# Performance work log

Hardware: AMD Instinct MI355X
Metric: run time of the kernel (lower is better)

The kernel has to match this reference:

```python
import jax, jax.numpy as jnp
import numpy as np

DIM = 96       # d_model / channels
DSTATE = 16    # SSM state size N
DINNER = 2 * DIM   # expand=2 -> 192
DTRANK = 6     # ceil(DIM/16)
K = 4          # scan directions
B, H, W = 2, 56, 56


def _ln(x, g, b, eps=1e-5):
    m = x.mean(-1, keepdims=True)
    v = x.var(-1, keepdims=True)
    return (x - m) * jax.lax.rsqrt(v + eps) * g + b


def _dwconv3(x, w, b):  # x [B,C,H,W], w [C,1,3,3] depthwise, SAME padding
    y = jax.lax.conv_general_dilated(x, w, (1, 1), [(1, 1), (1, 1)],
                                     feature_group_count=x.shape[1],
                                     dimension_numbers=('NCHW', 'OIHW', 'NCHW'))
    return y + b[None, :, None, None]


def _bn(x, g, b, m, v, eps=1e-5):  # eval-mode BatchNorm2d on NCHW
    inv = jax.lax.rsqrt(v + eps)
    return (x - m[None, :, None, None]) * (inv * g)[None, :, None, None] + b[None, :, None, None]


def _selective_scan(u, dt, A, Bs, Cs, Dp, dt_bias):
    # u, dt: [B,K,D,L]; A: [K,D,N]; Bs,Cs: [B,K,N,L]; Dp, dt_bias: [K,D]
    dt = jax.nn.softplus(dt + dt_bias[None, :, :, None])
    dA = jnp.exp(jnp.einsum('bkdl,kdn->lbkdn', dt, A))           # [L,B,K,D,N]
    dBu = jnp.einsum('bkdl,bknl,bkdl->lbkdn', dt, Bs, u)          # [L,B,K,D,N]
    Ct = jnp.moveaxis(Cs, -1, 0)                                  # [L,B,K,N]
    h0 = jnp.zeros(dA.shape[1:], dA.dtype)

    def step(h, inp):
        dA_l, dBu_l, C_l = inp
        h = dA_l * h + dBu_l
        return h, jnp.einsum('bkdn,bkn->bkd', h, C_l)

    _, ys = jax.lax.scan(step, h0, (dA, dBu, Ct))                 # ys [L,B,K,D]
    return jnp.moveaxis(ys, 0, -1) + u * Dp[None, :, :, None]     # [B,K,D,L]


def setup_inputs() -> dict:
    key = jax.random.key(0)
    ks = jax.random.split(key, 12)
    s = 0.02
    f32 = jnp.float32
    inp = {}
    inp['x'] = jax.random.normal(ks[0], (B, H, W, DIM), f32)
    # conv branch: depthwise 3x3 + BN + ReLU + 1x1 + BN
    inp['dw_w'] = jax.random.normal(ks[1], (DIM, 1, 3, 3), f32) * s
    inp['dw_b'] = jnp.zeros((DIM,), f32)
    inp['bn1_g'] = jnp.ones((DIM,), f32); inp['bn1_b'] = jnp.zeros((DIM,), f32)
    inp['bn1_m'] = jnp.zeros((DIM,), f32); inp['bn1_v'] = jnp.ones((DIM,), f32)
    inp['pw_w'] = jax.random.normal(ks[2], (DIM, DIM), f32) * s
    inp['pw_b'] = jnp.zeros((DIM,), f32)
    inp['bn2_g'] = jnp.ones((DIM,), f32); inp['bn2_b'] = jnp.zeros((DIM,), f32)
    inp['bn2_m'] = jnp.zeros((DIM,), f32); inp['bn2_v'] = jnp.ones((DIM,), f32)
    # pre-mamba LayerNorm
    inp['ln_g'] = jnp.ones((DIM,), f32); inp['ln_b'] = jnp.zeros((DIM,), f32)
    # SS2D params
    inp['in_proj_w'] = jax.random.normal(ks[3], (2 * DINNER, DIM), f32) * s
    inp['conv_w'] = jax.random.normal(ks[4], (DINNER, 1, 3, 3), f32) * s
    inp['conv_b'] = jnp.zeros((DINNER,), f32)
    inp['x_proj_w'] = jax.random.normal(ks[5], (K, DTRANK + 2 * DSTATE, DINNER), f32) * s
    inp['dt_w'] = jax.random.normal(ks[6], (K, DINNER, DTRANK), f32) * s
    inp['dt_b'] = jnp.full((K, DINNER), -4.6, f32)  # softplus(dt_b) ~= 0.01
    inp['A_logs'] = jnp.log(jnp.tile(jnp.arange(1, DSTATE + 1, dtype=f32), (K * DINNER, 1)))
    inp['Ds'] = jnp.ones((K * DINNER,), f32)
    inp['out_norm_g'] = jnp.ones((DINNER,), f32); inp['out_norm_b'] = jnp.zeros((DINNER,), f32)
    inp['out_proj_w'] = jax.random.normal(ks[7], (DIM, DINNER), f32) * s
    # fusion: Linear(2*dim, dim) + LayerNorm(dim)
    inp['fus_w'] = jax.random.normal(ks[8], (DIM, 2 * DIM), f32) * s
    inp['fus_b'] = jnp.zeros((DIM,), f32)
    inp['fus_ln_g'] = jnp.ones((DIM,), f32); inp['fus_ln_b'] = jnp.zeros((DIM,), f32)
    return inp


def reference(x, dw_w, dw_b, bn1_g, bn1_b, bn1_m, bn1_v, pw_w, pw_b,
              bn2_g, bn2_b, bn2_m, bn2_v, ln_g, ln_b,
              in_proj_w, conv_w, conv_b, x_proj_w, dt_w, dt_b, A_logs, Ds,
              out_norm_g, out_norm_b, out_proj_w, fus_w, fus_b, fus_ln_g, fus_ln_b):
    Bsz, Hh, Ww, C = x.shape
    L = Hh * Ww
    # ----- conv branch -----
    xc = jnp.transpose(x, (0, 3, 1, 2))                       # [B,C,H,W]
    c = jax.nn.relu(_bn(_dwconv3(xc, dw_w, dw_b), bn1_g, bn1_b, bn1_m, bn1_v))
    c = jnp.einsum('bchw,oc->bohw', c, pw_w) + pw_b[None, :, None, None]
    conv_out = jnp.transpose(_bn(c, bn2_g, bn2_b, bn2_m, bn2_v), (0, 2, 3, 1))
    # ----- mamba (SS2D) branch -----
    xn = _ln(x, ln_g, ln_b)
    xz = xn @ in_proj_w.T                                     # [B,H,W,2*Din]
    xm, z = jnp.split(xz, 2, axis=-1)
    xm = jnp.transpose(xm, (0, 3, 1, 2))                      # [B,Din,H,W]
    xm = jax.nn.silu(_dwconv3(xm, conv_w, conv_b))
    v1 = xm.reshape(Bsz, DINNER, L)                           # row-major scan
    v2 = jnp.transpose(xm, (0, 1, 3, 2)).reshape(Bsz, DINNER, L)  # col-major scan
    xs = jnp.stack([v1, v2, v1[..., ::-1], v2[..., ::-1]], axis=1)  # [B,4,Din,L]
    x_dbl = jnp.einsum('bkdl,kcd->bkcl', xs, x_proj_w)
    dts, Bmat, Cmat = jnp.split(x_dbl, [DTRANK, DTRANK + DSTATE], axis=2)
    dts = jnp.einsum('bkrl,kdr->bkdl', dts, dt_w)
    A = -jnp.exp(A_logs).reshape(K, DINNER, DSTATE)
    out_y = _selective_scan(xs, dts, A, Bmat, Cmat, Ds.reshape(K, DINNER), dt_b)
    y1 = out_y[:, 0]
    inv_y = out_y[:, 2:4][..., ::-1]
    y2 = inv_y[:, 0]
    y3 = jnp.transpose(inv_y[:, 1].reshape(Bsz, DINNER, Ww, Hh), (0, 1, 3, 2)).reshape(Bsz, DINNER, L)
    y4 = jnp.transpose(out_y[:, 1].reshape(Bsz, DINNER, Ww, Hh), (0, 1, 3, 2)).reshape(Bsz, DINNER, L)
    y = jnp.transpose(y1 + y2 + y3 + y4, (0, 2, 1)).reshape(Bsz, Hh, Ww, DINNER)
    y = _ln(y, out_norm_g, out_norm_b)
    y = y * jax.nn.silu(z)
    mamba_out = y @ out_proj_w.T                              # [B,H,W,C]
    # ----- fusion + residual -----
    fused = jnp.concatenate([conv_out, mamba_out], axis=-1) @ fus_w.T + fus_b
    fused = _ln(fused, fus_ln_g, fus_ln_b)
    return x + fused
```

## Files before the change

kernel.cpp:

```cpp
#include <hip/hip_runtime.h>
#include <math.h>

#define BZ 2
#define HH 56
#define WW 56
#define LL 3136
#define CC 96
#define DI 192
#define NS 16
#define RR 6
#define NT 49
#define NCH 98
#define CH 32

#define OFF_CONV   0
#define OFF_XMRAW  602112
#define OFF_Z      1806336
#define OFF_V1     3010560
#define OFF_V2     4214784
#define OFF_DT     5419008
#define OFF_BS     10235904
#define OFF_CS     10637312
#define OFF_Y      11038720
#define OFF_Y13    15855616
#define OFF_T      18264064
#define OFF_W2     19468288

__device__ __forceinline__ float softplusf(float x) {
    if (x > 20.f) return x;
    return log1pf(__expf(x));
}

__global__ __launch_bounds__(64) void k0_w2(const float* __restrict__ fus_w,
                                            const float* __restrict__ opw,
                                            float* __restrict__ W2) {
    int i = blockIdx.x * 64 + threadIdx.x;
    if (i >= CC * DI) return;
    int o = i / DI, d = i % DI;
    float acc = 0.f;
    for (int j = 0; j < CC; ++j)
        acc += fus_w[o * DI + CC + j] * opw[j * DI + d];
    W2[i] = acc;
}

__global__ __launch_bounds__(256) void k0c_negA(const float* __restrict__ A_logs,
                                                float* __restrict__ negA) {
    int i = blockIdx.x * 256 + threadIdx.x;
    if (i < 4 * DI * NS) negA[i] = -__expf(A_logs[i]);
}

__global__ __launch_bounds__(256) void k1a_dw(const float* __restrict__ x,
    const float* __restrict__ dw_w, const float* __restrict__ dw_b,
    const float* __restrict__ bn1_g, const float* __restrict__ bn1_b,
    const float* __restrict__ bn1_m, const float* __restrict__ bn1_v,
    float* __restrict__ cbuf) {
    int i = blockIdx.x * 256 + threadIdx.x;
    if (i >= BZ * LL * CC) return;
    int c = i % CC;
    int bl = i / CC;
    int l = bl % LL, b = bl / LL;
    int h = l / WW, w = l % WW;
    float acc = dw_b[c];
    #pragma unroll
    for (int dy = -1; dy <= 1; ++dy) {
        int hh = h + dy; if (hh < 0 || hh >= HH) continue;
        #pragma unroll
        for (int dx = -1; dx <= 1; ++dx) {
            int ww = w + dx; if (ww < 0 || ww >= WW) continue;
            acc += x[((b * HH + hh) * WW + ww) * CC + c] * dw_w[c * 9 + (dy + 1) * 3 + (dx + 1)];
        }
    }
    float inv = rsqrtf(bn1_v[c] + 1e-5f);
    float v = (acc - bn1_m[c]) * inv * bn1_g[c] + bn1_b[c];
    cbuf[i] = fmaxf(v, 0.f);
}

__global__ __launch_bounds__(256) void k1b_pw(const float* __restrict__ cbuf,
    const float* __restrict__ pw_w, const float* __restrict__ pw_b,
    const float* __restrict__ bn2_g, const float* __restrict__ bn2_b,
    const float* __restrict__ bn2_m, const float* __restrict__ bn2_v,
    float* __restrict__ conv_out) {
    int t0 = blockIdx.x * 64;
    int og = blockIdx.y;
    int b = blockIdx.z;
    int lane = threadIdx.x & 63;
    int wvu = __builtin_amdgcn_readfirstlane(threadIdx.x >> 6);
    __shared__ float ct[CC * 65];
    __shared__ float res[64 * 49];
    const float* cb = cbuf + (b * LL + t0) * CC;
    for (int e = threadIdx.x; e < 64 * CC; e += 256) {
        int p = e / CC, c = e % CC;
        ct[c * 65 + p] = cb[e];
    }
    __syncthreads();
    int o0 = og * 48 + wvu * 12;
    float acc[12];
    const float* pb = pw_b + o0;
    #pragma unroll
    for (int j = 0; j < 12; ++j) acc[j] = pb[j];
    const float* wb = pw_w + o0 * CC;
    for (int c = 0; c < CC; ++c) {
        float xv = ct[c * 65 + lane];
        #pragma unroll
        for (int j = 0; j < 12; ++j)
            acc[j] += xv * wb[j * CC + c];
    }
    #pragma unroll
    for (int j = 0; j < 12; ++j) {
        int o = o0 + j;
        float inv = rsqrtf(bn2_v[o] + 1e-5f);
        res[lane * 49 + wvu * 12 + j] = (acc[j] - bn2_m[o]) * inv * bn2_g[o] + bn2_b[o];
    }
    __syncthreads();
    float* ob = conv_out + (b * LL + t0) * CC + og * 48;
    for (int e = threadIdx.x; e < 64 * 48; e += 256) {
        int pl = e / 48, o = e % 48;
        ob[pl * CC + o] = res[pl * 49 + o];
    }
}

__global__ __launch_bounds__(256) void k2_inproj(const float* __restrict__ x,
    const float* __restrict__ ln_g, const float* __restrict__ ln_b,
    const float* __restrict__ ipw,
    float* __restrict__ xm_raw, float* __restrict__ z_buf) {
    int t0 = blockIdx.x * 64;
    int og = blockIdx.y;
    int b = blockIdx.z;
    int lane = threadIdx.x & 63;
    int wv = threadIdx.x >> 6;
    int wvu = __builtin_amdgcn_readfirstlane(wv);
    __shared__ float xt[64 * 97];
    __shared__ float xn[96 * 65];
    __shared__ float ps[4][64], ps2[4][64];
    const float* xb = x + (b * LL + t0) * CC;
    for (int e = threadIdx.x; e < 64 * CC; e += 256) {
        int p = e / CC, c = e % CC;
        xt[p * 97 + c] = xb[e];
    }
    __syncthreads();
    float s = 0.f, s2 = 0.f;
    #pragma unroll
    for (int j = 0; j < 24; ++j) {
        float v = xt[lane * 97 + wvu * 24 + j];
        s += v; s2 += v * v;
    }
    ps[wv][lane] = s; ps2[wv][lane] = s2;
    __syncthreads();
    float st = 0.f, st2 = 0.f;
    #pragma unroll
    for (int i = 0; i < 4; ++i) { st += ps[i][lane]; st2 += ps2[i][lane]; }
    float m = st * (1.f / 96.f);
    float inv = rsqrtf(st2 * (1.f / 96.f) - m * m + 1e-5f);
    #pragma unroll
    for (int j = 0; j < 24; ++j) {
        int c = wvu * 24 + j;
        xn[c * 65 + lane] = (xt[lane * 97 + c] - m) * inv * ln_g[c] + ln_b[c];
    }
    __syncthreads();
    float acc[12];
    #pragma unroll
    for (int j = 0; j < 12; ++j) acc[j] = 0.f;
    int o0 = og * 48 + wvu * 12;
    const float* wbase = ipw + o0 * CC;
    for (int c = 0; c < CC; ++c) {
        float xv = xn[c * 65 + lane];
        #pragma unroll
        for (int j = 0; j < 12; ++j)
            acc[j] += xv * wbase[j * CC + c];
    }
    int p = t0 + lane;
    #pragma unroll
    for (int j = 0; j < 12; ++j) {
        int out = o0 + j;
        if (out < DI) xm_raw[(b * DI + out) * LL + p] = acc[j];
        else          z_buf[(b * DI + (out - DI)) * LL + p] = acc[j];
    }
}

__global__ __launch_bounds__(256) void k3_dw(const float* __restrict__ xm_raw,
    const float* __restrict__ conv_w, const float* __restrict__ conv_b,
    float* __restrict__ v1, float* __restrict__ v2) {
    int bd = blockIdx.x;
    int half = blockIdx.y;
    int d = bd % DI;
    int h0 = half * 28;
    __shared__ float tile[28 * 57];
    const float* src = xm_raw + bd * LL;
    float wloc[9];
    #pragma unroll
    for (int i = 0; i < 9; ++i) wloc[i] = conv_w[d * 9 + i];
    float bias = conv_b[d];
    for (int e = threadIdx.x; e < 28 * WW; e += 256) {
        int hl = e / WW, w = e % WW;
        int h = h0 + hl;
        float acc = bias;
        #pragma unroll
        for (int dy = -1; dy <= 1; ++dy) {
            int hh = h + dy; if (hh < 0 || hh >= HH) continue;
            #pragma unroll
            for (int dx = -1; dx <= 1; ++dx) {
                int ww = w + dx; if (ww < 0 || ww >= WW) continue;
                acc += src[hh * WW + ww] * wloc[(dy + 1) * 3 + (dx + 1)];
            }
        }
        float sig = 1.f / (1.f + __expf(-acc));
        float v = acc * sig;
        v1[bd * LL + h * WW + w] = v;
        tile[hl * 57 + w] = v;
    }
    __syncthreads();
    for (int e = threadIdx.x; e < 28 * WW; e += 256) {
        int w = e / 28, hl = e % 28;
        v2[bd * LL + w * HH + h0 + hl] = tile[hl * 57 + w];
    }
}

__global__ __launch_bounds__(256) void k4a_xproj(const float* __restrict__ v1,
    const float* __restrict__ v2, const float* __restrict__ xpw,
    float* __restrict__ dtr_g, float* __restrict__ B_s, float* __restrict__ C_s) {
    int tile = blockIdx.x;
    int k = blockIdx.y, b = blockIdx.z;
    int lane = threadIdx.x & 63;
    int wvu = __builtin_amdgcn_readfirstlane(threadIdx.x >> 6);
    int t0 = tile * 64;
    int r0 = wvu * 10; if (r0 > 28) r0 = 28;
    const float* src = ((k & 1) == 0 ? v1 : v2) + b * DI * LL + t0;
    float acc[10];
    #pragma unroll
    for (int i = 0; i < 10; ++i) acc[i] = 0.f;
    const float* wbase = xpw + (k * 38 + r0) * DI;
    for (int d = 0; d < DI; ++d) {
        float xv = src[d * LL + lane];
        #pragma unroll
        for (int i = 0; i < 10; ++i)
            acc[i] += xv * wbase[i * DI + d];
    }
    int bk = b * 4 + k;
    int p = t0 + lane;
    #pragma unroll
    for (int i = 0; i < 10; ++i) {
        int c = r0 + i;
        if (c < RR) {
            dtr_g[(bk * RR + c) * LL + p] = acc[i];
        } else if (c < RR + NS) {
            B_s[(bk * NS + (c - RR)) * LL + p] = acc[i];
        } else {
            C_s[(bk * NS + (c - RR - NS)) * LL + p] = acc[i];
        }
    }
}

__global__ __launch_bounds__(256) void k4b_dt(const float* __restrict__ dtr_g,
    const float* __restrict__ dtw, const float* __restrict__ dtb,
    float* __restrict__ dt_s) {
    int t0 = blockIdx.x * 64;
    int k = blockIdx.y, b = blockIdx.z;
    int lane = threadIdx.x & 63;
    int wvu = __builtin_amdgcn_readfirstlane(threadIdx.x >> 6);
    int bk = b * 4 + k;
    int p = t0 + lane;
    float r[RR];
    #pragma unroll
    for (int i = 0; i < RR; ++i) r[i] = dtr_g[(bk * RR + i) * LL + p];
    for (int i = 0; i < 48; ++i) {
        int d = wvu * 48 + i;
        float a = dtb[k * DI + d];
        const float* wr = dtw + (k * DI + d) * RR;
        #pragma unroll
        for (int q = 0; q < RR; ++q)
            a += r[q] * wr[q];
        dt_s[(bk * DI + d) * LL + p] = softplusf(a);
    }
}

__global__ __launch_bounds__(128) void k5a_scan(const float* __restrict__ dt_s,
    const float* __restrict__ B_s, const float* __restrict__ C_s,
    const float* __restrict__ v1, const float* __restrict__ v2,
    const float* __restrict__ A_logs, float* __restrict__ y_scan,
    float* __restrict__ hl_buf, float* __restrict__ Tbuf) {
    int bx = blockIdx.x;
    int dg = bx % 3, c = bx / 3;
    int k = blockIdx.y, b = blockIdx.z;
    int bk = b * 4 + k;
    int tid = threadIdx.x;
    int lane = tid & 63;
    int wvu = __builtin_amdgcn_readfirstlane(tid >> 6);
    int d0 = dg * 64, d = d0 + lane;
    bool fwd = (k < 2);
    int s0 = fwd ? c * CH : (LL - (c + 1) * CH);
    __shared__ float dtl[64 * 33];
    __shared__ float ul[64 * 33];
    __shared__ float bc[CH * 36];
    float Ae[8];
    const float* ap = A_logs + (k * DI + d) * NS + wvu * 8;
    #pragma unroll
    for (int n = 0; n < 8; ++n) Ae[n] = -__expf(ap[n]) * 1.442695040888963f;
    const float* dtp = dt_s + (bk * DI + d0) * LL + s0;
    const float* up  = ((k & 1) == 0 ? v1 : v2) + (b * DI + d0) * LL + s0;
    int pr = tid >> 5, pc = tid & 31;
    int si = fwd ? pc : (31 - pc);
    #pragma unroll
    for (int i = 0; i < 16; ++i) {
        int row = i * 4 + pr;
        dtl[row * 33 + si] = dtp[row * LL + pc];
        ul[row * 33 + si]  = up[row * LL + pc];
    }
    #pragma unroll
    for (int i = 0; i < 4; ++i) {
        int nn = i * 4 + pr;
        bc[si * 36 + nn]      = B_s[(bk * NS + nn) * LL + s0 + pc];
        bc[si * 36 + 16 + nn] = C_s[(bk * NS + nn) * LL + s0 + pc];
    }
    __syncthreads();
    float h[8];
    #pragma unroll
    for (int n = 0; n < 8; ++n) h[n] = 0.f;
    float cum = 0.f;
    float yv_[CH];
    #pragma unroll
    for (int j = 0; j < CH; ++j) {
        float dtv = dtl[lane * 33 + j];
        float uv  = ul[lane * 33 + j];
        float du = dtv * uv;
        cum += dtv;
        const float* rb = &bc[j * 36 + wvu * 8];
        const float* rc = &bc[j * 36 + 16 + wvu * 8];
        float4 b0 = *(const float4*)rb, b1 = *(const float4*)(rb + 4);
        float4 c0 = *(const float4*)rc, c1 = *(const float4*)(rc + 4);
        float bv[8] = {b0.x, b0.y, b0.z, b0.w, b1.x, b1.y, b1.z, b1.w};
        float cv[8] = {c0.x, c0.y, c0.z, c0.w, c1.x, c1.y, c1.z, c1.w};
        float y = 0.f;
        #pragma unroll
        for (int n = 0; n < 8; ++n) {
            h[n] = exp2f(dtv * Ae[n]) * h[n] + du * bv[n];
            y += h[n] * cv[n];
        }
        yv_[j] = y;
    }
    __syncthreads();
    if (wvu == 0) {
        #pragma unroll
        for (int j = 0; j < CH; ++j) dtl[lane * 33 + j] = yv_[j];
    } else {
        #pragma unroll
        for (int j = 0; j < CH; ++j) ul[lane * 33 + j] = yv_[j];
    }
    __syncthreads();
    float* yp = y_scan + (bk * DI + d0) * LL + s0;
    #pragma unroll
    for (int i = 0; i < 16; ++i) {
        int row = i * 4 + pr;
        yp[row * LL + pc] = dtl[row * 33 + si] + ul[row * 33 + si];
    }
    float4* hp4 = (float4*)(hl_buf + (bk * NCH + c) * (DI * NS) + d * NS + wvu * 8);
    hp4[0] = make_float4(h[0], h[1], h[2], h[3]);
    hp4[1] = make_float4(h[4], h[5], h[6], h[7]);
    if (wvu == 0) Tbuf[(bk * NCH + c) * DI + d] = cum;
}

__global__ __launch_bounds__(64) void k5c_comb(float* __restrict__ hl_buf,
    const float* __restrict__ Tbuf, const float* __restrict__ negA) {
    int dg = blockIdx.x, k = blockIdx.y, b = blockIdx.z;
    int lane = threadIdx.x, dl = lane >> 4, n = lane & 15;
    int d = dg * 4 + dl;
    int bk = b * 4 + k;
    float Av = negA[(k * DI + d) * NS + n];
    float H = 0.f;
    float* slot0 = hl_buf + (bk * NCH + 0) * (DI * NS) + dg * 64 + lane;
    float hl_next = *slot0;
    float T_next = Tbuf[(bk * NCH + 0) * DI + d];
    for (int c = 0; c < NCH; ++c) {
        float hl = hl_next, T = T_next;
        if (c + 1 < NCH) {
            hl_next = hl_buf[(bk * NCH + c + 1) * (DI * NS) + dg * 64 + lane];
            T_next  = Tbuf[(bk * NCH + c + 1) * DI + d];
        }
        hl_buf[(bk * NCH + c) * (DI * NS) + dg * 64 + lane] = H;
        H = hl + __expf(Av * T) * H;
    }
}

__global__ __launch_bounds__(256) void k5d_corr(const float* __restrict__ dt_s,
    const float* __restrict__ C_s, const float* __restrict__ hin,
    const float* __restrict__ negA, float* __restrict__ y_scan) {
    int t = blockIdx.x;
    int k = blockIdx.y, b = blockIdx.z;
    bool fwd = (k < 2);
    int c  = fwd ? (t + 1) : (NCH - 1 - t);
    int s0 = fwd ? (t + 1) * CH : t * CH;
    int p32 = threadIdx.x & 31, sl = threadIdx.x >> 5;
    int bk = b * 4 + k;
    __shared__ float c_l[16 * 33];
    for (int e = threadIdx.x; e < 16 * CH; e += 256) {
        int n = e >> 5, s = e & 31;
        c_l[n * 33 + s] = C_s[(bk * NS + n) * LL + s0 + s];
    }
    __syncthreads();
    for (int j = 0; j < 24; ++j) {
        int d = sl * 24 + j;
        float dtv = dt_s[(bk * DI + d) * LL + s0 + p32];
        float cum = dtv;
        if (fwd) {
            #pragma unroll
            for (int off = 1; off < 32; off <<= 1) {
                float o = __shfl_up(cum, off, 32);
                if (p32 >= off) cum += o;
            }
        } else {
            #pragma unroll
            for (int off = 1; off < 32; off <<= 1) {
                float o = __shfl_down(cum, off, 32);
                if (p32 < 32 - off) cum += o;
            }
        }
        const float* hp = hin + (bk * NCH + c) * (DI * NS) + d * 16;
        const float* ap = negA + (k * DI + d) * NS;
        float acc = 0.f;
        #pragma unroll
        for (int n = 0; n < 16; ++n) {
            acc += c_l[n * 33 + p32] * __expf(ap[n] * cum) * hp[n];
        }
        y_scan[(bk * DI + d) * LL + s0 + p32] += acc;
    }
}

__global__ __launch_bounds__(256) void k5b_tr(const float* __restrict__ y_scan,
                                              float* __restrict__ y13t) {
    int idx = blockIdx.x;
    int d = idx % DI;
    int bk = idx / DI;
    int kk = bk % 2, b = bk / 2;
    int k = (kk == 0) ? 1 : 3;
    __shared__ float tile[HH * 57];
    const float* src = y_scan + ((b * 4 + k) * DI + d) * LL;
    for (int e = threadIdx.x; e < LL; e += 256) {
        int w = e / HH, h = e % HH;
        tile[h * 57 + w] = src[e];
    }
    __syncthreads();
    float* dst = y13t + idx * LL;
    for (int e = threadIdx.x; e < LL; e += 256) {
        int h = e / WW, w = e % WW;
        dst[e] = tile[h * 57 + w];
    }
}

__global__ __launch_bounds__(256) void k6_gather(const float* __restrict__ y_scan,
    const float* __restrict__ y13t, const float* __restrict__ v1,
    const float* __restrict__ z_buf, const float* __restrict__ Ds,
    const float* __restrict__ ong, const float* __restrict__ onb,
    float* __restrict__ t_buf) {
    int t0 = blockIdx.x * 16;
    int b = blockIdx.y;
    int p16 = threadIdx.x & 15, sl = threadIdx.x >> 4;
    int p = t0 + p16;
    __shared__ float yv[DI * 17];
    __shared__ float ps[16][16], ps2[16][16];
    float s = 0.f, s2 = 0.f;
    for (int j = 0; j < 12; ++j) {
        int d = sl * 12 + j;
        float dsum = Ds[d] + Ds[DI + d] + Ds[2 * DI + d] + Ds[3 * DI + d];
        float val = y_scan[((b * 4 + 0) * DI + d) * LL + p]
                  + y_scan[((b * 4 + 2) * DI + d) * LL + p]
                  + y13t[((b * 2 + 0) * DI + d) * LL + p]
                  + y13t[((b * 2 + 1) * DI + d) * LL + p]
                  + v1[(b * DI + d) * LL + p] * dsum;
        yv[d * 17 + p16] = val;
        s += val; s2 += val * val;
    }
    ps[sl][p16] = s; ps2[sl][p16] = s2;
    __syncthreads();
    float st = 0.f, st2 = 0.f;
    #pragma unroll
    for (int i = 0; i < 16; ++i) { st += ps[i][p16]; st2 += ps2[i][p16]; }
    float m = st * (1.f / 192.f);
    float inv = rsqrtf(st2 * (1.f / 192.f) - m * m + 1e-5f);
    for (int j = 0; j < 12; ++j) {
        int d = sl * 12 + j;
        float val = (yv[d * 17 + p16] - m) * inv * ong[d] + onb[d];
        float zz = z_buf[(b * DI + d) * LL + p];
        float sig = 1.f / (1.f + __expf(-zz));
        t_buf[(b * DI + d) * LL + p] = val * zz * sig;
    }
}

__global__ __launch_bounds__(256) void k7a_mm(const float* __restrict__ t_buf,
    const float* __restrict__ conv_out, const float* __restrict__ W2,
    const float* __restrict__ fus_w, const float* __restrict__ fus_b,
    float* __restrict__ fusedT) {
    int t0 = blockIdx.x * 64;
    int og = blockIdx.y;
    int b = blockIdx.z;
    int lane = threadIdx.x & 63;
    int wvu = __builtin_amdgcn_readfirstlane(threadIdx.x >> 6);
    __shared__ float ct[CC * 65];
    const float* cb = conv_out + (b * LL + t0) * CC;
    for (int e = threadIdx.x; e < 64 * CC; e += 256) {
        int p = e / CC, c = e % CC;
        ct[c * 65 + p] = cb[e];
    }
    __syncthreads();
    int o0 = og * 12 + wvu * 3;
    float acc[3];
    #pragma unroll
    for (int j = 0; j < 3; ++j) acc[j] = fus_b[o0 + j];
    int p = t0 + lane;
    const float* w2 = W2 + o0 * DI;
    for (int d = 0; d < DI; ++d) {
        float tv = t_buf[(b * DI + d) * LL + p];
        #pragma unroll
        for (int j = 0; j < 3; ++j)
            acc[j] += tv * w2[j * DI + d];
    }
    const float* fw = fus_w + o0 * DI;
    for (int c = 0; c < CC; ++c) {
        float cv = ct[c * 65 + lane];
        #pragma unroll
        for (int j = 0; j < 3; ++j)
            acc[j] += cv * fw[j * DI + c];
    }
    #pragma unroll
    for (int j = 0; j < 3; ++j)
        fusedT[(b * CC + o0 + j) * LL + p] = acc[j];
}

__global__ __launch_bounds__(256) void k7b_ln(const float* __restrict__ fusedT,
    const float* __restrict__ flg, const float* __restrict__ flb,
    const float* __restrict__ x, float* __restrict__ out) {
    int t0 = blockIdx.x * 16;
    int b = blockIdx.y;
    int p16 = threadIdx.x & 15, sl = threadIdx.x >> 4;
    __shared__ float ft[CC * 17];
    __shared__ float res[16 * 97];
    __shared__ float ps[16][16], ps2[16][16];
    for (int e = threadIdx.x; e < CC * 16; e += 256) {
        int o = e >> 4, p = e & 15;
        ft[o * 17 + p] = fusedT[(b * CC + o) * LL + t0 + p];
    }
    __syncthreads();
    float s = 0.f, s2 = 0.f;
    #pragma unroll
    for (int j = 0; j < 6; ++j) {
        float v = ft[(sl * 6 + j) * 17 + p16];
        s += v; s2 += v * v;
    }
    ps[sl][p16] = s; ps2[sl][p16] = s2;
    __syncthreads();
    float st = 0.f, st2 = 0.f;
    #pragma unroll
    for (int i = 0; i < 16; ++i) { st += ps[i][p16]; st2 += ps2[i][p16]; }
    float m = st * (1.f / 96.f);
    float inv = rsqrtf(st2 * (1.f / 96.f) - m * m + 1e-5f);
    #pragma unroll
    for (int j = 0; j < 6; ++j) {
        int o = sl * 6 + j;
        res[p16 * 97 + o] = (ft[o * 17 + p16] - m) * inv * flg[o] + flb[o];
    }
    __syncthreads();
    const float* xb = x + (b * LL + t0) * CC;
    float* ob = out + (b * LL + t0) * CC;
    for (int e = threadIdx.x; e < 16 * CC; e += 256) {
        int pl = e / CC, o = e % CC;
        ob[e] = xb[e] + res[pl * 97 + o];
    }
}

extern "C" void kernel_launch(void* const* d_in, const int* in_sizes, int n_in,
                              void* d_out, int out_size, void* d_ws, size_t ws_size,
                              hipStream_t stream) {
    const float* x        = (const float*)d_in[0];
    const float* dw_w     = (const float*)d_in[1];
    const float* dw_b     = (const float*)d_in[2];
    const float* bn1_g    = (const float*)d_in[3];
    const float* bn1_b    = (const float*)d_in[4];
    const float* bn1_m    = (const float*)d_in[5];
    const float* bn1_v    = (const float*)d_in[6];
    const float* pw_w     = (const float*)d_in[7];
    const float* pw_b     = (const float*)d_in[8];
    const float* bn2_g    = (const float*)d_in[9];
    const float* bn2_b    = (const float*)d_in[10];
    const float* bn2_m    = (const float*)d_in[11];
    const float* bn2_v    = (const float*)d_in[12];
    const float* ln_g     = (const float*)d_in[13];
    const float* ln_b     = (const float*)d_in[14];
    const float* ipw      = (const float*)d_in[15];
    const float* conv_w   = (const float*)d_in[16];
    const float* conv_b   = (const float*)d_in[17];
    const float* xpw      = (const float*)d_in[18];
    const float* dtw      = (const float*)d_in[19];
    const float* dtb      = (const float*)d_in[20];
    const float* A_logs   = (const float*)d_in[21];
    const float* Ds       = (const float*)d_in[22];
    const float* ong      = (const float*)d_in[23];
    const float* onb      = (const float*)d_in[24];
    const float* opw      = (const float*)d_in[25];
    const float* fus_w    = (const float*)d_in[26];
    const float* fus_b    = (const float*)d_in[27];
    const float* flg      = (const float*)d_in[28];
    const float* flb      = (const float*)d_in[29];

    float* ws = (float*)d_ws;
    float* conv_out = ws + OFF_CONV;
    float* xm_raw   = ws + OFF_XMRAW;
    float* z_buf    = ws + OFF_Z;
    float* v1       = ws + OFF_V1;
    float* v2       = ws + OFF_V2;
    float* dt_s     = ws + OFF_DT;
    float* B_s      = ws + OFF_BS;
    float* C_s      = ws + OFF_CS;
    float* y_scan   = ws + OFF_Y;
    float* y13t     = ws + OFF_Y13;
    float* t_buf    = ws + OFF_T;
    float* W2       = ws + OFF_W2;
    float* cbuf     = y13t;
    float* hl_buf   = y13t;
    float* Tbuf     = xm_raw;
    float* dtr_g    = xm_raw + 262144;
    float* negA     = B_s;
    float* fusedT   = y13t;
    float* out      = (float*)d_out;

    k0_w2<<<dim3((CC * DI + 63) / 64), dim3(64), 0, stream>>>(fus_w, opw, W2);
    k1a_dw<<<dim3((BZ * LL * CC + 255) / 256), dim3(256), 0, stream>>>(x, dw_w, dw_b,
                                                     bn1_g, bn1_b, bn1_m, bn1_v, cbuf);
    k1b_pw<<<dim3(NT, 2, BZ), dim3(256), 0, stream>>>(cbuf, pw_w, pw_b,
                                                   bn2_g, bn2_b, bn2_m, bn2_v, conv_out);
    k2_inproj<<<dim3(NT, 8, BZ), dim3(256), 0, stream>>>(x, ln_g, ln_b, ipw, xm_raw, z_buf);
    k3_dw<<<dim3(BZ * DI, 2), dim3(256), 0, stream>>>(xm_raw, conv_w, conv_b, v1, v2);
    k4a_xproj<<<dim3(NT, 4, BZ), dim3(256), 0, stream>>>(v1, v2, xpw, dtr_g, B_s, C_s);
    k4b_dt<<<dim3(NT, 4, BZ), dim3(256), 0, stream>>>(dtr_g, dtw, dtb, dt_s);
    k5a_scan<<<dim3(3 * NCH, 4, BZ), dim3(128), 0, stream>>>(dt_s, B_s, C_s, v1, v2, A_logs,
                                                             y_scan, hl_buf, Tbuf);
    k0c_negA<<<dim3(48), dim3(256), 0, stream>>>(A_logs, negA);
    k5c_comb<<<dim3(48, 4, BZ), dim3(64), 0, stream>>>(hl_buf, Tbuf, negA);
    k5d_corr<<<dim3(NCH - 1, 4, BZ), dim3(256), 0, stream>>>(dt_s, C_s, hl_buf, negA, y_scan);
    k5b_tr<<<dim3(BZ * 2 * DI), dim3(256), 0, stream>>>(y_scan, y13t);
    k6_gather<<<dim3(196, BZ), dim3(256), 0, stream>>>(y_scan, y13t, v1, z_buf, Ds, ong, onb, t_buf);
    k7a_mm<<<dim3(NT, 8, BZ), dim3(256), 0, stream>>>(t_buf, conv_out, W2, fus_w, fus_b, fusedT);
    k7b_ln<<<dim3(196, BZ), dim3(256), 0, stream>>>(fusedT, flg, flb, x, out);
}
```

Measured before the change: 360.2 us.

## Vectorize scan-kernel staging with XOR-swizzled LDS and segmented output buffering

Rewrites the chunked selective-scan kernel's staging so that dt, u, B and C are loaded from global memory as float4 instead of scalars. The 33/36-float padding in LDS is replaced by XOR swizzles to avoid bank conflicts, and dt*u is precomputed during staging. The per-thread 32-element output buffer is split into four 8-step segments, each flushed to LDS behind an extra barrier, to lower register pressure; together with a launch_bounds occupancy hint this aims for higher occupancy. The final y store also becomes float4, at the cost of more barriers and swizzle index math.

```diff
diff --git a/kernel.cpp b/kernel.cpp
--- a/kernel.cpp
+++ b/kernel.cpp
@@ -273,7 +273,7 @@
     }
 }
 
-__global__ __launch_bounds__(128) void k5a_scan(const float* __restrict__ dt_s,
+__global__ __launch_bounds__(128, 4) void k5a_scan(const float* __restrict__ dt_s,
     const float* __restrict__ B_s, const float* __restrict__ C_s,
     const float* __restrict__ v1, const float* __restrict__ v2,
     const float* __restrict__ A_logs, float* __restrict__ y_scan,
@@ -288,69 +288,104 @@
     int d0 = dg * 64, d = d0 + lane;
     bool fwd = (k < 2);
     int s0 = fwd ? c * CH : (LL - (c + 1) * CH);
-    __shared__ float dtl[64 * 33];
-    __shared__ float ul[64 * 33];
-    __shared__ float bc[CH * 36];
+    __shared__ float dtl[64 * 32];
+    __shared__ float ul[64 * 32];
+    __shared__ alignas(16) float bc[32 * 32];
     float Ae[8];
     const float* ap = A_logs + (k * DI + d) * NS + wvu * 8;
     #pragma unroll
     for (int n = 0; n < 8; ++n) Ae[n] = -__expf(ap[n]) * 1.442695040888963f;
     const float* dtp = dt_s + (bk * DI + d0) * LL + s0;
     const float* up  = ((k & 1) == 0 ? v1 : v2) + (b * DI + d0) * LL + s0;
-    int pr = tid >> 5, pc = tid & 31;
-    int si = fwd ? pc : (31 - pc);
-    #pragma unroll
-    for (int i = 0; i < 16; ++i) {
-        int row = i * 4 + pr;
-        dtl[row * 33 + si] = dtp[row * LL + pc];
-        ul[row * 33 + si]  = up[row * LL + pc];
-    }
-    #pragma unroll
-    for (int i = 0; i < 4; ++i) {
-        int nn = i * 4 + pr;
-        bc[si * 36 + nn]      = B_s[(bk * NS + nn) * LL + s0 + pc];
-        bc[si * 36 + 16 + nn] = C_s[(bk * NS + nn) * LL + s0 + pc];
+    #pragma unroll
+    for (int q = 0; q < 4; ++q) {
+        int e = q * 128 + tid;
+        int row = e >> 3;
+        int p4 = (e & 7) << 2;
+        float4 dv = *(const float4*)(dtp + row * LL + p4);
+        float4 uv = *(const float4*)(up + row * LL + p4);
+        float dvv[4] = {dv.x, dv.y, dv.z, dv.w};
+        float uvv[4] = {uv.x, uv.y, uv.z, uv.w};
+        int rsw = row & 31;
+        #pragma unroll
+        for (int t = 0; t < 4; ++t) {
+            int s = fwd ? (p4 + t) : (31 - (p4 + t));
+            dtl[row * 32 + (s ^ rsw)] = dvv[t];
+            ul [row * 32 + (s ^ rsw)] = dvv[t] * uvv[t];
+        }
+    }
+    #pragma unroll
+    for (int q = 0; q < 2; ++q) {
+        int e = q * 128 + tid;
+        int row = e >> 3;
+        int p4 = (e & 7) << 2;
+        const float* src = (row < 16 ? B_s + (bk * NS + row) * LL
+                                     : C_s + (bk * NS + (row - 16)) * LL) + s0 + p4;
+        float4 v = *(const float4*)src;
+        float vv[4] = {v.x, v.y, v.z, v.w};
+        #pragma unroll
+        for (int t = 0; t < 4; ++t) {
+            int s = fwd ? (p4 + t) : (31 - (p4 + t));
+            bc[s * 32 + (row ^ ((s & 7) << 2))] = vv[t];
+        }
     }
     __syncthreads();
     float h[8];
     #pragma unroll
     for (int n = 0; n < 8; ++n) h[n] = 0.f;
     float cum = 0.f;
-    float yv_[CH];
-    #pragma unroll
-    for (int j = 0; j < CH; ++j) {
-        float dtv = dtl[lane * 33 + j];
-        float uv  = ul[lane * 33 + j];
-        float du = dtv * uv;
-        cum += dtv;
-        const float* rb = &bc[j * 36 + wvu * 8];
-        const float* rc = &bc[j * 36 + 16 + wvu * 8];
-        float4 b0 = *(const float4*)rb, b1 = *(const float4*)(rb + 4);
-        float4 c0 = *(const float4*)rc, c1 = *(const float4*)(rc + 4);
-        float bv[8] = {b0.x, b0.y, b0.z, b0.w, b1.x, b1.y, b1.z, b1.w};
-        float cv[8] = {c0.x, c0.y, c0.z, c0.w, c1.x, c1.y, c1.z, c1.w};
-        float y = 0.f;
-        #pragma unroll
-        for (int n = 0; n < 8; ++n) {
-            h[n] = exp2f(dtv * Ae[n]) * h[n] + du * bv[n];
-            y += h[n] * cv[n];
-        }
-        yv_[j] = y;
-    }
-    __syncthreads();
-    if (wvu == 0) {
-        #pragma unroll
-        for (int j = 0; j < CH; ++j) dtl[lane * 33 + j] = yv_[j];
-    } else {
-        #pragma unroll
-        for (int j = 0; j < CH; ++j) ul[lane * 33 + j] = yv_[j];
+    int lbase = lane * 32;
+    int lsw = lane & 31;
+    int w8 = wvu * 8;
+    #pragma unroll
+    for (int seg = 0; seg < 4; ++seg) {
+        float yv_[8];
+        #pragma unroll
+        for (int jj = 0; jj < 8; ++jj) {
+            int j = seg * 8 + jj;
+            float dtv = dtl[lbase + (j ^ lsw)];
+            float du  = ul [lbase + (j ^ lsw)];
+            cum += dtv;
+            int cswz = (j & 7) << 2;
+            const float* rb0 = &bc[j * 32 + ( w8       ^ cswz)];
+            const float* rb1 = &bc[j * 32 + ((w8 +  4) ^ cswz)];
+            const float* rc0 = &bc[j * 32 + ((w8 + 16) ^ cswz)];
+            const float* rc1 = &bc[j * 32 + ((w8 + 20) ^ cswz)];
+            float4 b0 = *(const float4*)rb0, b1 = *(const float4*)rb1;
+            float4 c0 = *(const float4*)rc0, c1 = *(const float4*)rc1;
+            float bv[8] = {b0.x, b0.y, b0.z, b0.w, b1.x, b1.y, b1.z, b1.w};
+            float cv[8] = {c0.x, c0.y, c0.z, c0.w, c1.x, c1.y, c1.z, c1.w};
+            float y = 0.f;
+            #pragma unroll
+            for (int n = 0; n < 8; ++n) {
+                h[n] = exp2f(dtv * Ae[n]) * h[n] + du * bv[n];
+                y += h[n] * cv[n];
+            }
+            yv_[jj] = y;
+        }
+        __syncthreads();
+        float* dst = (wvu == 0) ? dtl : ul;
+        #pragma unroll
+        for (int jj = 0; jj < 8; ++jj) {
+            int j = seg * 8 + jj;
+            dst[lbase + (j ^ lsw)] = yv_[jj];
+        }
     }
     __syncthreads();
     float* yp = y_scan + (bk * DI + d0) * LL + s0;
     #pragma unroll
-    for (int i = 0; i < 16; ++i) {
-        int row = i * 4 + pr;
-        yp[row * LL + pc] = dtl[row * 33 + si] + ul[row * 33 + si];
+    for (int q = 0; q < 4; ++q) {
+        int e = q * 128 + tid;
+        int row = e >> 3;
+        int p4 = (e & 7) << 2;
+        int rsw = row & 31;
+        float ov[4];
+        #pragma unroll
+        for (int t = 0; t < 4; ++t) {
+            int s = fwd ? (p4 + t) : (31 - (p4 + t));
+            ov[t] = dtl[row * 32 + (s ^ rsw)] + ul[row * 32 + (s ^ rsw)];
+        }
+        *(float4*)(yp + row * LL + p4) = make_float4(ov[0], ov[1], ov[2], ov[3]);
     }
     float4* hp4 = (float4*)(hl_buf + (bk * NCH + c) * (DI * NS) + d * NS + wvu * 8);
     hp4[0] = make_float4(h[0], h[1], h[2], h[3]);
```

Measured after the change: 357.2 us. No clear change (-0.8%).
